# Kernel optimization log

Hardware: AMD Instinct MI355X
Metric: run time of the kernel (lower is better)

The kernel has to match this reference:

```python
import jax, jax.numpy as jnp
import numpy as np

N = 50000      # nodes
E = 800000     # edges (before self loops)
IN = 256       # input feature dim
H = 4          # heads
C = 64         # hidden per head (concat=False -> mean over heads -> 64)
LAT = 32       # latent dim
ED = 3         # edge feature dim
NEG_SLOPE = 0.2


def setup_inputs() -> dict:
    key = jax.random.key(0)
    ks = jax.random.split(key, 24)
    nrm = lambda k, shp, s=0.05: jax.random.normal(k, shp, jnp.float32) * s
    inp = {
        'x': jax.random.normal(ks[0], (N, IN), jnp.float32),
        'edge_index': jax.random.randint(ks[1], (2, E), 0, N),
        'edge_attr': jax.random.normal(ks[2], (E, ED), jnp.float32),
    }
    i = 3
    for l, d in enumerate([IN, C]):  # layer 0 in_dim=IN, layer 1 in_dim=hidden
        inp[f'Wl{l}'] = nrm(ks[i], (d, H * C)); i += 1
        inp[f'bl{l}'] = jnp.zeros((H * C,), jnp.float32)
        inp[f'Wr{l}'] = nrm(ks[i], (d, H * C)); i += 1
        inp[f'br{l}'] = jnp.zeros((H * C,), jnp.float32)
        inp[f'We{l}'] = nrm(ks[i], (ED, H * C)); i += 1
        inp[f'att{l}'] = nrm(ks[i], (H, C)); i += 1
        inp[f'bias{l}'] = jnp.zeros((C,), jnp.float32)
    inp['Wmu'] = nrm(ks[i], (C, LAT)); i += 1
    inp['bmu'] = jnp.zeros((LAT,), jnp.float32)
    return inp


def _gatv2(x, edge_index, edge_attr, Wl, bl, Wr, br, We, att, bias):
    # PyG GATv2Conv: heads=H, concat=False, add_self_loops=True,
    # edge_dim=3, fill_value='mean', negative_slope=0.2, share_weights=False
    n = x.shape[0]
    src, dst = edge_index[0], edge_index[1]
    # self-loop edge_attr = mean of incoming edge_attr per node (0 if none)
    deg = jax.ops.segment_sum(jnp.ones((src.shape[0],), jnp.float32), dst, num_segments=n)
    loop_attr = jax.ops.segment_sum(edge_attr, dst, num_segments=n) / jnp.maximum(deg, 1.0)[:, None]
    loop = jnp.arange(n)
    s = jnp.concatenate([src, loop])
    d = jnp.concatenate([dst, loop])
    ea = jnp.concatenate([edge_attr, loop_attr], axis=0)
    xl = (x @ Wl + bl).reshape(n, H, C)   # source transform
    xr = (x @ Wr + br).reshape(n, H, C)   # target transform
    ee = (ea @ We).reshape(-1, H, C)      # edge transform (no bias)
    m = jax.nn.leaky_relu(xl[s] + xr[d] + ee, NEG_SLOPE)   # [Etot, H, C]
    alpha = jnp.einsum('ehc,hc->eh', m, att)                # [Etot, H]
    amax = jax.ops.segment_max(alpha, d, num_segments=n)    # per-dst max (all segments nonempty: self loops)
    ex = jnp.exp(alpha - amax[d])
    a = ex / jax.ops.segment_sum(ex, d, num_segments=n)[d]  # segment softmax
    out = jax.ops.segment_sum(xl[s] * a[:, :, None], d, num_segments=n)  # [N, H, C]
    return out.mean(axis=1) + bias  # concat=False -> head mean, then bias


def reference(x, edge_index, edge_attr,
              Wl0, bl0, Wr0, br0, We0, att0, bias0,
              Wl1, bl1, Wr1, br1, We1, att1, bias1,
              Wmu, bmu):
    h = jax.nn.relu(_gatv2(x, edge_index, edge_attr, Wl0, bl0, Wr0, br0, We0, att0, bias0))
    h = jax.nn.relu(_gatv2(h, edge_index, edge_attr, Wl1, bl1, Wr1, br1, We1, att1, bias1))
    return h @ Wmu + bmu
```

## Files before the change

kernel.cpp:

```cpp
#include <hip/hip_runtime.h>


#define NN  50000
#define EE  800000
#define HC  256
#define NSLOPE 0.2f

typedef float f32x4 __attribute__((ext_vector_type(4)));
typedef short bf16x8 __attribute__((ext_vector_type(8)));

__device__ __forceinline__ unsigned short f2b(float f) {
    unsigned u = __float_as_uint(f);
    u += 0x7FFFu + ((u >> 16) & 1u);
    return (unsigned short)(u >> 16);
}
__device__ __forceinline__ float b2f(unsigned short h) {
    return __uint_as_float((unsigned)h << 16);
}

__global__ __launch_bounds__(256) void deg_kernel(
    const int* __restrict__ dst, int* __restrict__ deg)
{
    int i = blockIdx.x * 256 + threadIdx.x;
    if (i >= EE / 4) return;
    int4 v = ((const int4*)dst)[i];
    atomicAdd(&deg[v.x], 1);
    atomicAdd(&deg[v.y], 1);
    atomicAdd(&deg[v.z], 1);
    atomicAdd(&deg[v.w], 1);
}

__global__ __launch_bounds__(1024) void scan_kernel(
    const int* __restrict__ deg, int* __restrict__ row_start, int* __restrict__ cursor)
{
    __shared__ int sums[1024];
    const int tid = threadIdx.x;
    const int CH = (NN + 1023) / 1024;
    int b = tid * CH, e = min(b + CH, NN);
    int s = 0;
    for (int i = b; i < e; i++) s += deg[i];
    sums[tid] = s;
    __syncthreads();
    for (int off = 1; off < 1024; off <<= 1) {
        int v = (tid >= off) ? sums[tid - off] : 0;
        __syncthreads();
        sums[tid] += v;
        __syncthreads();
    }
    int run = (tid == 0) ? 0 : sums[tid - 1];
    for (int i = b; i < e; i++) {
        row_start[i] = run;
        cursor[i]    = run;
        run += deg[i];
    }
    if (tid == 0) row_start[NN] = EE;
}

__global__ __launch_bounds__(256) void scatter_kernel(
    const int* __restrict__ ei, const float* __restrict__ ea,
    int* __restrict__ cursor, float4* __restrict__ csr)
{
    int i = blockIdx.x * 256 + threadIdx.x;
    if (i >= EE / 4) return;
    int4 s = ((const int4*)ei)[i];
    int4 d = ((const int4*)(ei + EE))[i];
    float4 e0 = ((const float4*)ea)[i * 3 + 0];
    float4 e1 = ((const float4*)ea)[i * 3 + 1];
    float4 e2 = ((const float4*)ea)[i * 3 + 2];
    int p0 = atomicAdd(&cursor[d.x], 1);
    int p1 = atomicAdd(&cursor[d.y], 1);
    int p2 = atomicAdd(&cursor[d.z], 1);
    int p3 = atomicAdd(&cursor[d.w], 1);
    csr[p0] = make_float4(__int_as_float(s.x), e0.x, e0.y, e0.z);
    csr[p1] = make_float4(__int_as_float(s.y), e0.w, e1.x, e1.y);
    csr[p2] = make_float4(__int_as_float(s.z), e1.z, e1.w, e2.x);
    csr[p3] = make_float4(__int_as_float(s.w), e2.y, e2.z, e2.w);
}

__global__ __launch_bounds__(256) void cvt_wt(
    const float* __restrict__ W, unsigned short* __restrict__ WTh,
    unsigned short* __restrict__ WTl, int K)
{
    int i = blockIdx.x * 256 + threadIdx.x;
    if (i >= K * 256) return;
    int k = i >> 8, c = i & 255;
    float v = W[i];
    unsigned short h = f2b(v);
    unsigned short l = f2b(v - b2f(h));
    WTh[(size_t)c * K + k] = h;
    WTl[(size_t)c * K + k] = l;
}

__global__ __launch_bounds__(256) void gemm_fused(
    const float* __restrict__ A,
    const unsigned short* __restrict__ BTh, const unsigned short* __restrict__ BTl,
    const float* __restrict__ bias0, const float* __restrict__ bias1,
    float* __restrict__ C0, float* __restrict__ C1,
    int M, int K)
{
    __shared__ unsigned short Ah[64][36], Al[64][36];
    __shared__ unsigned short Bh[256][36], Bl[256][36];
    const int tid = threadIdx.x;
    const int bm = blockIdx.y << 6;
    const int bn = blockIdx.x << 8;
    const int w  = tid >> 6, l = tid & 63;
    const int wr = w >> 1, wc = w & 1;
    const int lr = l & 15, lk = l >> 4;

    f32x4 acc[2][8];
#pragma unroll
    for (int a = 0; a < 2; a++)
#pragma unroll
        for (int b = 0; b < 8; b++) acc[a][b] = (f32x4){0.f, 0.f, 0.f, 0.f};

    const int ar = tid >> 2, ac = (tid & 3) << 3;

    for (int k0 = 0; k0 < K; k0 += 32) {
        float av[8];
        if (bm + ar < M) {
            *(float4*)&av[0] = *(const float4*)&A[(size_t)(bm + ar) * K + k0 + ac];
            *(float4*)&av[4] = *(const float4*)&A[(size_t)(bm + ar) * K + k0 + ac + 4];
        } else {
#pragma unroll
            for (int j = 0; j < 8; j++) av[j] = 0.f;
        }
        unsigned hp[4], lp[4];
#pragma unroll
        for (int j = 0; j < 4; j++) {
            unsigned short h0 = f2b(av[2 * j]),     h1 = f2b(av[2 * j + 1]);
            unsigned short l0 = f2b(av[2 * j]     - b2f(h0));
            unsigned short l1 = f2b(av[2 * j + 1] - b2f(h1));
            hp[j] = (unsigned)h0 | ((unsigned)h1 << 16);
            lp[j] = (unsigned)l0 | ((unsigned)l1 << 16);
        }
        *(uint4*)&Ah[ar][ac] = make_uint4(hp[0], hp[1], hp[2], hp[3]);
        *(uint4*)&Al[ar][ac] = make_uint4(lp[0], lp[1], lp[2], lp[3]);
#pragma unroll
        for (int rep = 0; rep < 4; rep++) {
            int i  = (rep << 8) + tid;
            int rb = i >> 2, cb = (i & 3) << 3;
            *(uint4*)&Bh[rb][cb] = *(const uint4*)&BTh[(size_t)(bn + rb) * K + k0 + cb];
            *(uint4*)&Bl[rb][cb] = *(const uint4*)&BTl[(size_t)(bn + rb) * K + k0 + cb];
        }
        __syncthreads();

        bf16x8 afh[2], afl[2];
#pragma unroll
        for (int a = 0; a < 2; a++) {
            afh[a] = *(const bf16x8*)&Ah[wr * 32 + a * 16 + lr][lk << 3];
            afl[a] = *(const bf16x8*)&Al[wr * 32 + a * 16 + lr][lk << 3];
        }
#pragma unroll
        for (int b = 0; b < 8; b++) {
            bf16x8 bh = *(const bf16x8*)&Bh[wc * 128 + b * 16 + lr][lk << 3];
            bf16x8 bl_ = *(const bf16x8*)&Bl[wc * 128 + b * 16 + lr][lk << 3];
#pragma unroll
            for (int a = 0; a < 2; a++) {
                acc[a][b] = __builtin_amdgcn_mfma_f32_16x16x32_bf16(afh[a], bh,  acc[a][b], 0, 0, 0);
                acc[a][b] = __builtin_amdgcn_mfma_f32_16x16x32_bf16(afh[a], bl_, acc[a][b], 0, 0, 0);
                acc[a][b] = __builtin_amdgcn_mfma_f32_16x16x32_bf16(afl[a], bh,  acc[a][b], 0, 0, 0);
            }
        }
        __syncthreads();
    }

    const float* bias = (bn == 0) ? bias0 : bias1;
    float* C = (bn == 0) ? C0 : C1;
#pragma unroll
    for (int a = 0; a < 2; a++) {
        int rbase = bm + wr * 32 + a * 16 + (lk << 2);
#pragma unroll
        for (int b = 0; b < 8; b++) {
            int c = wc * 128 + b * 16 + lr;
            float bs = bias[c];
#pragma unroll
            for (int i = 0; i < 4; i++) {
                int rg = rbase + i;
                if (rg < M) C[(size_t)rg * HC + c] = acc[a][b][i] + bs;
            }
        }
    }
}

__global__ __launch_bounds__(256) void gat_edge(
    const float* __restrict__ xl, const float* __restrict__ xr,
    const float4* __restrict__ csr, const int* __restrict__ row_start,
    const float* __restrict__ att, const float* __restrict__ We,
    const float* __restrict__ bias, float* __restrict__ out)
{
    const int lane = threadIdx.x & 63;
    const int wid  = (blockIdx.x * 256 + threadIdx.x) >> 6;
    const int base = wid << 2;
    const int j4 = lane << 2;
    const float4* xlv = (const float4*)xl;

    const float4 at4 = *(const float4*)&att[j4];
    const float4 w0  = *(const float4*)&We[j4];
    const float4 w1  = *(const float4*)&We[HC + j4];
    const float4 w2  = *(const float4*)&We[2 * HC + j4];

#pragma unroll 1
    for (int v = 0; v < 4; v++) {
        const int node = base + v;
        const float4 xr4 = *(const float4*)&xr[(size_t)node * HC + j4];

        float acc0 = 0.f, acc1 = 0.f, acc2 = 0.f, acc3 = 0.f, denom = 0.f;
        float eas0 = 0.f, eas1 = 0.f, eas2 = 0.f;
        const int beg = row_start[node];
        const int n   = row_start[node + 1] - beg;
        const float4* cp = csr + beg;

        float4 r0 = {0,0,0,0}, r1 = {0,0,0,0}, r2 = {0,0,0,0};
        float4 v0 = {0,0,0,0}, v1 = {0,0,0,0};
        if (n > 0) { r0 = cp[0]; v0 = xlv[(size_t)__float_as_int(r0.x) * 64 + lane]; }
        if (n > 1) { r1 = cp[1]; v1 = xlv[(size_t)__float_as_int(r1.x) * 64 + lane]; }
        if (n > 2) { r2 = cp[2]; }

        for (int i = 0; i < n; i++) {
            float4 crec = r0, cxv = v0;
            r0 = r1; r1 = r2; v0 = v1;
            if (i + 3 < n) r2 = cp[i + 3];
            if (i + 2 < n) v1 = xlv[(size_t)__float_as_int(r1.x) * 64 + lane];

            float ea0 = crec.y, ea1 = crec.z, ea2 = crec.w;
            eas0 += ea0; eas1 += ea1; eas2 += ea2;
            float m0 = cxv.x + xr4.x + ea0 * w0.x + ea1 * w1.x + ea2 * w2.x;
            float m1 = cxv.y + xr4.y + ea0 * w0.y + ea1 * w1.y + ea2 * w2.y;
            float m2 = cxv.z + xr4.z + ea0 * w0.z + ea1 * w1.z + ea2 * w2.z;
            float m3 = cxv.w + xr4.w + ea0 * w0.w + ea1 * w1.w + ea2 * w2.w;
            m0 = fmaxf(m0, NSLOPE * m0);
            m1 = fmaxf(m1, NSLOPE * m1);
            m2 = fmaxf(m2, NSLOPE * m2);
            m3 = fmaxf(m3, NSLOPE * m3);
            float p = m0 * at4.x + m1 * at4.y + m2 * at4.z + m3 * at4.w;
            p += __shfl_xor(p, 1);
            p += __shfl_xor(p, 2);
            p += __shfl_xor(p, 4);
            p += __shfl_xor(p, 8);
            float ex = __expf(p);
            denom += ex;
            acc0 = fmaf(ex, cxv.x, acc0);
            acc1 = fmaf(ex, cxv.y, acc1);
            acc2 = fmaf(ex, cxv.z, acc2);
            acc3 = fmaf(ex, cxv.w, acc3);
        }

        {
            float rd = 1.0f / fmaxf((float)n, 1.0f);
            float ea0 = eas0 * rd, ea1 = eas1 * rd, ea2 = eas2 * rd;
            float4 sv = xlv[(size_t)node * 64 + lane];
            float m0 = sv.x + xr4.x + ea0 * w0.x + ea1 * w1.x + ea2 * w2.x;
            float m1 = sv.y + xr4.y + ea0 * w0.y + ea1 * w1.y + ea2 * w2.y;
            float m2 = sv.z + xr4.z + ea0 * w0.z + ea1 * w1.z + ea2 * w2.z;
            float m3 = sv.w + xr4.w + ea0 * w0.w + ea1 * w1.w + ea2 * w2.w;
            m0 = fmaxf(m0, NSLOPE * m0);
            m1 = fmaxf(m1, NSLOPE * m1);
            m2 = fmaxf(m2, NSLOPE * m2);
            m3 = fmaxf(m3, NSLOPE * m3);
            float p = m0 * at4.x + m1 * at4.y + m2 * at4.z + m3 * at4.w;
            p += __shfl_xor(p, 1);
            p += __shfl_xor(p, 2);
            p += __shfl_xor(p, 4);
            p += __shfl_xor(p, 8);
            float ex = __expf(p);
            denom += ex;
            acc0 = fmaf(ex, sv.x, acc0);
            acc1 = fmaf(ex, sv.y, acc1);
            acc2 = fmaf(ex, sv.z, acc2);
            acc3 = fmaf(ex, sv.w, acc3);
        }

        const float inv = 1.0f / denom;
        float r0s = acc0 * inv, r1s = acc1 * inv, r2s = acc2 * inv, r3s = acc3 * inv;
        r0s += __shfl_xor(r0s, 16); r0s += __shfl_xor(r0s, 32);
        r1s += __shfl_xor(r1s, 16); r1s += __shfl_xor(r1s, 32);
        r2s += __shfl_xor(r2s, 16); r2s += __shfl_xor(r2s, 32);
        r3s += __shfl_xor(r3s, 16); r3s += __shfl_xor(r3s, 32);
        if (lane < 16) {
            float4 bv = *(const float4*)&bias[j4];
            float4 o;
            o.x = fmaxf(0.25f * r0s + bv.x, 0.f);
            o.y = fmaxf(0.25f * r1s + bv.y, 0.f);
            o.z = fmaxf(0.25f * r2s + bv.z, 0.f);
            o.w = fmaxf(0.25f * r3s + bv.w, 0.f);
            *(float4*)&out[(size_t)node * 64 + j4] = o;
        }
    }
}

__global__ __launch_bounds__(256) void mu_kernel(
    const float* __restrict__ h, const float* __restrict__ Wmu,
    const float* __restrict__ bmu, float* __restrict__ out)
{
    __shared__ float ws[64 * 32];
    __shared__ float hs[8 * 64];
    const int tid = threadIdx.x;
#pragma unroll
    for (int i = 0; i < 8; i++) ws[tid + i * 256] = Wmu[tid + i * 256];
    const int nb = blockIdx.x * 8;
    {
        int idx = tid * 2;
        *(float2*)&hs[idx] = *(const float2*)&h[(size_t)nb * 64 + idx];
    }
    __syncthreads();
    const int ln = tid >> 5;
    const int o  = tid & 31;
    float acc = bmu[o];
#pragma unroll
    for (int k = 0; k < 64; k++) acc = fmaf(hs[ln * 64 + k], ws[k * 32 + o], acc);
    out[(size_t)(nb + ln) * 32 + o] = acc;
}

extern "C" void kernel_launch(void* const* d_in, const int* in_sizes, int n_in,
                              void* d_out, int out_size, void* d_ws, size_t ws_size,
                              hipStream_t stream) {
    const float* x    = (const float*)d_in[0];
    const int*   ei   = (const int*)  d_in[1];
    const float* ea   = (const float*)d_in[2];
    const float* Wl0  = (const float*)d_in[3];
    const float* bl0  = (const float*)d_in[4];
    const float* Wr0  = (const float*)d_in[5];
    const float* br0  = (const float*)d_in[6];
    const float* We0  = (const float*)d_in[7];
    const float* att0 = (const float*)d_in[8];
    const float* bi0  = (const float*)d_in[9];
    const float* Wl1  = (const float*)d_in[10];
    const float* bl1  = (const float*)d_in[11];
    const float* Wr1  = (const float*)d_in[12];
    const float* br1  = (const float*)d_in[13];
    const float* We1  = (const float*)d_in[14];
    const float* att1 = (const float*)d_in[15];
    const float* bi1  = (const float*)d_in[16];
    const float* Wmu  = (const float*)d_in[17];
    const float* bmu  = (const float*)d_in[18];
    float* out = (float*)d_out;

    float* xl32 = (float*)d_ws;
    float* xr32 = xl32 + (size_t)NN * HC;
    float* h1   = xr32 + (size_t)NN * HC;
    int*   deg  = (int*)(h1 + (size_t)NN * 64);
    int*   rows = deg + NN;
    int*   curs = rows + NN + 1;
    uintptr_t p = (uintptr_t)(curs + NN);
    p = (p + 15) & ~(uintptr_t)15;
    unsigned short* WT0h = (unsigned short*)p;
    unsigned short* WT0l = WT0h + 512 * 256;
    unsigned short* WT1h = WT0l + 512 * 256;
    unsigned short* WT1l = WT1h + 512 * 64;
    p = (uintptr_t)(WT1l + 512 * 64);
    p = (p + 255) & ~(uintptr_t)255;
    float4* csr = (float4*)p;

    hipMemsetAsync(deg, 0, NN * sizeof(int), stream);
    deg_kernel<<<(EE / 4 + 255) / 256, 256, 0, stream>>>(ei + EE, deg);
    scan_kernel<<<1, 1024, 0, stream>>>(deg, rows, curs);
    scatter_kernel<<<(EE / 4 + 255) / 256, 256, 0, stream>>>(ei, ea, curs, csr);

    cvt_wt<<<256, 256, 0, stream>>>(Wl0, WT0h,             WT0l,             256);
    cvt_wt<<<256, 256, 0, stream>>>(Wr0, WT0h + 256 * 256, WT0l + 256 * 256, 256);
    cvt_wt<<< 64, 256, 0, stream>>>(Wl1, WT1h,             WT1l,             64);
    cvt_wt<<< 64, 256, 0, stream>>>(Wr1, WT1h + 256 * 64,  WT1l + 256 * 64,  64);

    dim3 gg(2, (NN + 63) / 64);
    const int gat_grid = NN / 16;

    gemm_fused<<<gg, 256, 0, stream>>>(x, WT0h, WT0l, bl0, br0, xl32, xr32, NN, 256);
    gat_edge<<<gat_grid, 256, 0, stream>>>(xl32, xr32, csr, rows, att0, We0, bi0, h1);

    gemm_fused<<<gg, 256, 0, stream>>>(h1, WT1h, WT1l, bl1, br1, xl32, xr32, NN, 64);
    gat_edge<<<gat_grid, 256, 0, stream>>>(xl32, xr32, csr, rows, att1, We1, bi1, h1);

    mu_kernel<<<NN / 8, 256, 0, stream>>>(h1, Wmu, bmu, out);
}
```

Before: 727.8 us.

## Remap GAT edge kernel to one node per wave with four edges in flight

The edge-aggregation kernel now assigns one destination node per wavefront instead of four nodes processed in sequence. The wave is split into four 16-lane groups that each handle a different incoming edge, and each lane covers 16 channels loaded as four vectors. Partial softmax sums and edge-attribute means are combined across groups with shuffles before the self-loop term, then reduced across heads. The aim is more memory-level parallelism for the gathered source rows and fewer shuffles per edge. The cost is higher register pressure and some idle lanes on the last partial iteration for low-degree nodes.

```diff
diff --git a/kernel.cpp b/kernel.cpp
--- a/kernel.cpp
+++ b/kernel.cpp
@@ -152,7 +152,7 @@
         }
 #pragma unroll
         for (int b = 0; b < 8; b++) {
-            bf16x8 bh = *(const bf16x8*)&Bh[wc * 128 + b * 16 + lr][lk << 3];
+            bf16x8 bh  = *(const bf16x8*)&Bh[wc * 128 + b * 16 + lr][lk << 3];
             bf16x8 bl_ = *(const bf16x8*)&Bl[wc * 128 + b * 16 + lr][lk << 3];
 #pragma unroll
             for (int a = 0; a < 2; a++) {
@@ -189,101 +189,144 @@
     const float* __restrict__ bias, float* __restrict__ out)
 {
     const int lane = threadIdx.x & 63;
-    const int wid  = (blockIdx.x * 256 + threadIdx.x) >> 6;
-    const int base = wid << 2;
-    const int j4 = lane << 2;
-    const float4* xlv = (const float4*)xl;
-
-    const float4 at4 = *(const float4*)&att[j4];
-    const float4 w0  = *(const float4*)&We[j4];
-    const float4 w1  = *(const float4*)&We[HC + j4];
-    const float4 w2  = *(const float4*)&We[2 * HC + j4];
-
-#pragma unroll 1
-    for (int v = 0; v < 4; v++) {
-        const int node = base + v;
-        const float4 xr4 = *(const float4*)&xr[(size_t)node * HC + j4];
-
-        float acc0 = 0.f, acc1 = 0.f, acc2 = 0.f, acc3 = 0.f, denom = 0.f;
-        float eas0 = 0.f, eas1 = 0.f, eas2 = 0.f;
-        const int beg = row_start[node];
-        const int n   = row_start[node + 1] - beg;
-        const float4* cp = csr + beg;
-
-        float4 r0 = {0,0,0,0}, r1 = {0,0,0,0}, r2 = {0,0,0,0};
-        float4 v0 = {0,0,0,0}, v1 = {0,0,0,0};
-        if (n > 0) { r0 = cp[0]; v0 = xlv[(size_t)__float_as_int(r0.x) * 64 + lane]; }
-        if (n > 1) { r1 = cp[1]; v1 = xlv[(size_t)__float_as_int(r1.x) * 64 + lane]; }
-        if (n > 2) { r2 = cp[2]; }
-
-        for (int i = 0; i < n; i++) {
-            float4 crec = r0, cxv = v0;
-            r0 = r1; r1 = r2; v0 = v1;
-            if (i + 3 < n) r2 = cp[i + 3];
-            if (i + 2 < n) v1 = xlv[(size_t)__float_as_int(r1.x) * 64 + lane];
-
-            float ea0 = crec.y, ea1 = crec.z, ea2 = crec.w;
-            eas0 += ea0; eas1 += ea1; eas2 += ea2;
-            float m0 = cxv.x + xr4.x + ea0 * w0.x + ea1 * w1.x + ea2 * w2.x;
-            float m1 = cxv.y + xr4.y + ea0 * w0.y + ea1 * w1.y + ea2 * w2.y;
-            float m2 = cxv.z + xr4.z + ea0 * w0.z + ea1 * w1.z + ea2 * w2.z;
-            float m3 = cxv.w + xr4.w + ea0 * w0.w + ea1 * w1.w + ea2 * w2.w;
-            m0 = fmaxf(m0, NSLOPE * m0);
-            m1 = fmaxf(m1, NSLOPE * m1);
-            m2 = fmaxf(m2, NSLOPE * m2);
-            m3 = fmaxf(m3, NSLOPE * m3);
-            float p = m0 * at4.x + m1 * at4.y + m2 * at4.z + m3 * at4.w;
-            p += __shfl_xor(p, 1);
-            p += __shfl_xor(p, 2);
-            p += __shfl_xor(p, 4);
-            p += __shfl_xor(p, 8);
-            float ex = __expf(p);
-            denom += ex;
-            acc0 = fmaf(ex, cxv.x, acc0);
-            acc1 = fmaf(ex, cxv.y, acc1);
-            acc2 = fmaf(ex, cxv.z, acc2);
-            acc3 = fmaf(ex, cxv.w, acc3);
-        }
-
-        {
-            float rd = 1.0f / fmaxf((float)n, 1.0f);
-            float ea0 = eas0 * rd, ea1 = eas1 * rd, ea2 = eas2 * rd;
-            float4 sv = xlv[(size_t)node * 64 + lane];
-            float m0 = sv.x + xr4.x + ea0 * w0.x + ea1 * w1.x + ea2 * w2.x;
-            float m1 = sv.y + xr4.y + ea0 * w0.y + ea1 * w1.y + ea2 * w2.y;
-            float m2 = sv.z + xr4.z + ea0 * w0.z + ea1 * w1.z + ea2 * w2.z;
-            float m3 = sv.w + xr4.w + ea0 * w0.w + ea1 * w1.w + ea2 * w2.w;
-            m0 = fmaxf(m0, NSLOPE * m0);
-            m1 = fmaxf(m1, NSLOPE * m1);
-            m2 = fmaxf(m2, NSLOPE * m2);
-            m3 = fmaxf(m3, NSLOPE * m3);
-            float p = m0 * at4.x + m1 * at4.y + m2 * at4.z + m3 * at4.w;
-            p += __shfl_xor(p, 1);
-            p += __shfl_xor(p, 2);
-            p += __shfl_xor(p, 4);
-            p += __shfl_xor(p, 8);
-            float ex = __expf(p);
-            denom += ex;
-            acc0 = fmaf(ex, sv.x, acc0);
-            acc1 = fmaf(ex, sv.y, acc1);
-            acc2 = fmaf(ex, sv.z, acc2);
-            acc3 = fmaf(ex, sv.w, acc3);
-        }
-
-        const float inv = 1.0f / denom;
-        float r0s = acc0 * inv, r1s = acc1 * inv, r2s = acc2 * inv, r3s = acc3 * inv;
-        r0s += __shfl_xor(r0s, 16); r0s += __shfl_xor(r0s, 32);
-        r1s += __shfl_xor(r1s, 16); r1s += __shfl_xor(r1s, 32);
-        r2s += __shfl_xor(r2s, 16); r2s += __shfl_xor(r2s, 32);
-        r3s += __shfl_xor(r3s, 16); r3s += __shfl_xor(r3s, 32);
-        if (lane < 16) {
-            float4 bv = *(const float4*)&bias[j4];
-            float4 o;
-            o.x = fmaxf(0.25f * r0s + bv.x, 0.f);
-            o.y = fmaxf(0.25f * r1s + bv.y, 0.f);
-            o.z = fmaxf(0.25f * r2s + bv.z, 0.f);
-            o.w = fmaxf(0.25f * r3s + bv.w, 0.f);
-            *(float4*)&out[(size_t)node * 64 + j4] = o;
+    const int node = (blockIdx.x * 256 + threadIdx.x) >> 6;
+    if (node >= NN) return;
+    const int g = lane >> 4;
+    const int j = lane & 15;
+    const f32x4* xlv = (const f32x4*)xl;
+    const int cb4 = j << 2;
+
+    f32x4 w0[4], w1[4], w2[4], at[4], xr4[4];
+#pragma unroll
+    for (int q = 0; q < 4; q++) {
+        w0[q]  = *(const f32x4*)&We[        (cb4 + q) * 4];
+        w1[q]  = *(const f32x4*)&We[HC     + (cb4 + q) * 4];
+        w2[q]  = *(const f32x4*)&We[2 * HC + (cb4 + q) * 4];
+        at[q]  = *(const f32x4*)&att[       (cb4 + q) * 4];
+        xr4[q] = xlv[0];
+    }
+    {
+        const f32x4* xrv = (const f32x4*)xr;
+#pragma unroll
+        for (int q = 0; q < 4; q++) xr4[q] = xrv[(size_t)node * 64 + cb4 + q];
+    }
+
+    f32x4 acc[4];
+#pragma unroll
+    for (int q = 0; q < 4; q++) acc[q] = (f32x4){0.f, 0.f, 0.f, 0.f};
+    float denom = 0.f, eas0 = 0.f, eas1 = 0.f, eas2 = 0.f;
+
+    const int beg = row_start[node];
+    const int n   = row_start[node + 1] - beg;
+    const float4* cp = csr + beg;
+    const int nit = (n + 3) >> 2;
+
+    int idx = g;
+    bool val = idx < n;
+    float4 rec = val ? cp[idx] : make_float4(0.f, 0.f, 0.f, 0.f);
+    f32x4 xv0, xv1, xv2, xv3;
+    {
+        int s = val ? __float_as_int(rec.x) : node;
+        const f32x4* gp = xlv + (size_t)s * 64 + cb4;
+        xv0 = gp[0]; xv1 = gp[1]; xv2 = gp[2]; xv3 = gp[3];
+    }
+
+    for (int it = 0; it < nit; it++) {
+        const bool  cv = val;
+        const float4 crec = rec;
+        f32x4 c0 = xv0, c1 = xv1, c2 = xv2, c3 = xv3;
+        idx += 4;
+        val = idx < n;
+        if (val) {
+            rec = cp[idx];
+            const f32x4* gp = xlv + (size_t)__float_as_int(rec.x) * 64 + cb4;
+            xv0 = gp[0]; xv1 = gp[1]; xv2 = gp[2]; xv3 = gp[3];
+        } else {
+            rec = make_float4(0.f, 0.f, 0.f, 0.f);
+        }
+
+        const float ea0 = crec.y, ea1 = crec.z, ea2 = crec.w;
+        eas0 += ea0; eas1 += ea1; eas2 += ea2;
+
+        float p = 0.f;
+        f32x4 cx[4] = {c0, c1, c2, c3};
+#pragma unroll
+        for (int q = 0; q < 4; q++) {
+            f32x4 m = cx[q] + xr4[q];
+            m += ea0 * w0[q];
+            m += ea1 * w1[q];
+            m += ea2 * w2[q];
+#pragma unroll
+            for (int t = 0; t < 4; t++) m[t] = fmaxf(m[t], NSLOPE * m[t]);
+#pragma unroll
+            for (int t = 0; t < 4; t++) p = fmaf(m[t], at[q][t], p);
+            cx[q] = m;
+        }
+        p += __shfl_xor(p, 1);
+        p += __shfl_xor(p, 2);
+        float ex = cv ? __expf(p) : 0.f;
+        denom += ex;
+        acc[0] += ex * c0;
+        acc[1] += ex * c1;
+        acc[2] += ex * c2;
+        acc[3] += ex * c3;
+    }
+
+    float* af = (float*)acc;
+#pragma unroll
+    for (int k = 0; k < 16; k++) {
+        af[k] += __shfl_xor(af[k], 16);
+        af[k] += __shfl_xor(af[k], 32);
+    }
+    denom += __shfl_xor(denom, 16); denom += __shfl_xor(denom, 32);
+    eas0  += __shfl_xor(eas0, 16);  eas0  += __shfl_xor(eas0, 32);
+    eas1  += __shfl_xor(eas1, 16);  eas1  += __shfl_xor(eas1, 32);
+    eas2  += __shfl_xor(eas2, 16);  eas2  += __shfl_xor(eas2, 32);
+
+    {
+        const float rd = 1.0f / fmaxf((float)n, 1.0f);
+        const float ea0 = eas0 * rd, ea1 = eas1 * rd, ea2 = eas2 * rd;
+        const f32x4* gp = xlv + (size_t)node * 64 + cb4;
+        f32x4 sv[4] = {gp[0], gp[1], gp[2], gp[3]};
+        float p = 0.f;
+#pragma unroll
+        for (int q = 0; q < 4; q++) {
+            f32x4 m = sv[q] + xr4[q];
+            m += ea0 * w0[q];
+            m += ea1 * w1[q];
+            m += ea2 * w2[q];
+#pragma unroll
+            for (int t = 0; t < 4; t++) m[t] = fmaxf(m[t], NSLOPE * m[t]);
+#pragma unroll
+            for (int t = 0; t < 4; t++) p = fmaf(m[t], at[q][t], p);
+        }
+        p += __shfl_xor(p, 1);
+        p += __shfl_xor(p, 2);
+        float ex = __expf(p);
+        denom += ex;
+        acc[0] += ex * sv[0];
+        acc[1] += ex * sv[1];
+        acc[2] += ex * sv[2];
+        acc[3] += ex * sv[3];
+    }
+
+    const float inv = 1.0f / denom;
+#pragma unroll
+    for (int k = 0; k < 16; k++) {
+        float r = af[k] * inv;
+        r += __shfl_xor(r, 4);
+        r += __shfl_xor(r, 8);
+        af[k] = r;
+    }
+    if (lane < 4) {
+        const f32x4* bv = (const f32x4*)bias;
+        f32x4* ov = (f32x4*)out;
+#pragma unroll
+        for (int q = 0; q < 4; q++) {
+            f32x4 o = 0.25f * acc[q] + bv[cb4 + q];
+#pragma unroll
+            for (int t = 0; t < 4; t++) o[t] = fmaxf(o[t], 0.f);
+            ov[(size_t)node * 16 + cb4 + q] = o;
         }
     }
 }
@@ -362,7 +405,7 @@
     cvt_wt<<< 64, 256, 0, stream>>>(Wr1, WT1h + 256 * 64,  WT1l + 256 * 64,  64);
 
     dim3 gg(2, (NN + 63) / 64);
-    const int gat_grid = NN / 16;
+    const int gat_grid = (NN * 64) / 256;
 
     gemm_fused<<<gg, 256, 0, stream>>>(x, WT0h, WT0l, bl0, br0, xl32, xr32, NN, 256);
     gat_edge<<<gat_grid, 256, 0, stream>>>(xl32, xr32, csr, rows, att0, We0, bi0, h1);
```

After: 782.1 us. +7.5%, slower.

## Parallelize CSR prefix scan across blocks and assign one wave per node

Applied to the files above, without the earlier changes.

Replaces the single-block serial-chunk prefix scan over node degrees with a three-kernel multi-block scan. The GAT edge kernel now gives each wavefront one destination node instead of looping over four, which quadruples the grid and gives the scheduler more waves to hide gather latency. Index arithmetic for xl gathers is switched to 32-bit unsigned. The trade-off is two extra kernel launches and redundant per-wave loads of att/We.

```diff
diff --git a/kernel.cpp b/kernel.cpp
--- a/kernel.cpp
+++ b/kernel.cpp
@@ -5,6 +5,7 @@
 #define EE  800000
 #define HC  256
 #define NSLOPE 0.2f
+#define SCAN_B ((NN + 255) / 256)
 
 typedef float f32x4 __attribute__((ext_vector_type(4)));
 typedef short bf16x8 __attribute__((ext_vector_type(8)));
@@ -30,30 +31,52 @@
     atomicAdd(&deg[v.w], 1);
 }
 
-__global__ __launch_bounds__(1024) void scan_kernel(
-    const int* __restrict__ deg, int* __restrict__ row_start, int* __restrict__ cursor)
-{
-    __shared__ int sums[1024];
-    const int tid = threadIdx.x;
-    const int CH = (NN + 1023) / 1024;
-    int b = tid * CH, e = min(b + CH, NN);
-    int s = 0;
-    for (int i = b; i < e; i++) s += deg[i];
-    sums[tid] = s;
+__global__ __launch_bounds__(256) void scan1_kernel(
+    const int* __restrict__ deg, int* __restrict__ rows, int* __restrict__ bsum)
+{
+    __shared__ int sh[256];
+    const int t = threadIdx.x, b = blockIdx.x;
+    const int i = b * 256 + t;
+    int v = (i < NN) ? deg[i] : 0;
+    sh[t] = v;
     __syncthreads();
-    for (int off = 1; off < 1024; off <<= 1) {
-        int v = (tid >= off) ? sums[tid - off] : 0;
-        __syncthreads();
-        sums[tid] += v;
-        __syncthreads();
-    }
-    int run = (tid == 0) ? 0 : sums[tid - 1];
-    for (int i = b; i < e; i++) {
-        row_start[i] = run;
-        cursor[i]    = run;
-        run += deg[i];
-    }
-    if (tid == 0) row_start[NN] = EE;
+    for (int off = 1; off < 256; off <<= 1) {
+        int u = (t >= off) ? sh[t - off] : 0;
+        __syncthreads();
+        sh[t] += u;
+        __syncthreads();
+    }
+    if (i < NN) rows[i] = sh[t] - v;
+    if (t == 255) bsum[b] = sh[255];
+}
+
+__global__ __launch_bounds__(256) void scan2_kernel(int* __restrict__ bsum, int* __restrict__ boff)
+{
+    __shared__ int sh[256];
+    const int t = threadIdx.x;
+    int v = (t < SCAN_B) ? bsum[t] : 0;
+    sh[t] = v;
+    __syncthreads();
+    for (int off = 1; off < 256; off <<= 1) {
+        int u = (t >= off) ? sh[t - off] : 0;
+        __syncthreads();
+        sh[t] += u;
+        __syncthreads();
+    }
+    if (t < SCAN_B) boff[t] = sh[t] - v;
+}
+
+__global__ __launch_bounds__(256) void scan3_kernel(
+    int* __restrict__ rows, int* __restrict__ curs, const int* __restrict__ boff)
+{
+    const int b = blockIdx.x;
+    const int i = b * 256 + threadIdx.x;
+    if (i < NN) {
+        int v = rows[i] + boff[b];
+        rows[i] = v;
+        curs[i] = v;
+    }
+    if (i == 0) rows[NN] = EE;
 }
 
 __global__ __launch_bounds__(256) void scatter_kernel(
@@ -152,7 +175,7 @@
         }
 #pragma unroll
         for (int b = 0; b < 8; b++) {
-            bf16x8 bh = *(const bf16x8*)&Bh[wc * 128 + b * 16 + lr][lk << 3];
+            bf16x8 bh  = *(const bf16x8*)&Bh[wc * 128 + b * 16 + lr][lk << 3];
             bf16x8 bl_ = *(const bf16x8*)&Bl[wc * 128 + b * 16 + lr][lk << 3];
 #pragma unroll
             for (int a = 0; a < 2; a++) {
@@ -189,102 +212,97 @@
     const float* __restrict__ bias, float* __restrict__ out)
 {
     const int lane = threadIdx.x & 63;
-    const int wid  = (blockIdx.x * 256 + threadIdx.x) >> 6;
-    const int base = wid << 2;
+    const int node = (blockIdx.x * 256 + threadIdx.x) >> 6;
+    if (node >= NN) return;
     const int j4 = lane << 2;
     const float4* xlv = (const float4*)xl;
 
+    const float4 xr4 = *(const float4*)&xr[(size_t)node * HC + j4];
     const float4 at4 = *(const float4*)&att[j4];
     const float4 w0  = *(const float4*)&We[j4];
     const float4 w1  = *(const float4*)&We[HC + j4];
     const float4 w2  = *(const float4*)&We[2 * HC + j4];
 
-#pragma unroll 1
-    for (int v = 0; v < 4; v++) {
-        const int node = base + v;
-        const float4 xr4 = *(const float4*)&xr[(size_t)node * HC + j4];
-
-        float acc0 = 0.f, acc1 = 0.f, acc2 = 0.f, acc3 = 0.f, denom = 0.f;
-        float eas0 = 0.f, eas1 = 0.f, eas2 = 0.f;
-        const int beg = row_start[node];
-        const int n   = row_start[node + 1] - beg;
-        const float4* cp = csr + beg;
-
-        float4 r0 = {0,0,0,0}, r1 = {0,0,0,0}, r2 = {0,0,0,0};
-        float4 v0 = {0,0,0,0}, v1 = {0,0,0,0};
-        if (n > 0) { r0 = cp[0]; v0 = xlv[(size_t)__float_as_int(r0.x) * 64 + lane]; }
-        if (n > 1) { r1 = cp[1]; v1 = xlv[(size_t)__float_as_int(r1.x) * 64 + lane]; }
-        if (n > 2) { r2 = cp[2]; }
-
-        for (int i = 0; i < n; i++) {
-            float4 crec = r0, cxv = v0;
-            r0 = r1; r1 = r2; v0 = v1;
-            if (i + 3 < n) r2 = cp[i + 3];
-            if (i + 2 < n) v1 = xlv[(size_t)__float_as_int(r1.x) * 64 + lane];
-
-            float ea0 = crec.y, ea1 = crec.z, ea2 = crec.w;
-            eas0 += ea0; eas1 += ea1; eas2 += ea2;
-            float m0 = cxv.x + xr4.x + ea0 * w0.x + ea1 * w1.x + ea2 * w2.x;
-            float m1 = cxv.y + xr4.y + ea0 * w0.y + ea1 * w1.y + ea2 * w2.y;
-            float m2 = cxv.z + xr4.z + ea0 * w0.z + ea1 * w1.z + ea2 * w2.z;
-            float m3 = cxv.w + xr4.w + ea0 * w0.w + ea1 * w1.w + ea2 * w2.w;
-            m0 = fmaxf(m0, NSLOPE * m0);
-            m1 = fmaxf(m1, NSLOPE * m1);
-            m2 = fmaxf(m2, NSLOPE * m2);
-            m3 = fmaxf(m3, NSLOPE * m3);
-            float p = m0 * at4.x + m1 * at4.y + m2 * at4.z + m3 * at4.w;
-            p += __shfl_xor(p, 1);
-            p += __shfl_xor(p, 2);
-            p += __shfl_xor(p, 4);
-            p += __shfl_xor(p, 8);
-            float ex = __expf(p);
-            denom += ex;
-            acc0 = fmaf(ex, cxv.x, acc0);
-            acc1 = fmaf(ex, cxv.y, acc1);
-            acc2 = fmaf(ex, cxv.z, acc2);
-            acc3 = fmaf(ex, cxv.w, acc3);
-        }
-
-        {
-            float rd = 1.0f / fmaxf((float)n, 1.0f);
-            float ea0 = eas0 * rd, ea1 = eas1 * rd, ea2 = eas2 * rd;
-            float4 sv = xlv[(size_t)node * 64 + lane];
-            float m0 = sv.x + xr4.x + ea0 * w0.x + ea1 * w1.x + ea2 * w2.x;
-            float m1 = sv.y + xr4.y + ea0 * w0.y + ea1 * w1.y + ea2 * w2.y;
-            float m2 = sv.z + xr4.z + ea0 * w0.z + ea1 * w1.z + ea2 * w2.z;
-            float m3 = sv.w + xr4.w + ea0 * w0.w + ea1 * w1.w + ea2 * w2.w;
-            m0 = fmaxf(m0, NSLOPE * m0);
-            m1 = fmaxf(m1, NSLOPE * m1);
-            m2 = fmaxf(m2, NSLOPE * m2);
-            m3 = fmaxf(m3, NSLOPE * m3);
-            float p = m0 * at4.x + m1 * at4.y + m2 * at4.z + m3 * at4.w;
-            p += __shfl_xor(p, 1);
-            p += __shfl_xor(p, 2);
-            p += __shfl_xor(p, 4);
-            p += __shfl_xor(p, 8);
-            float ex = __expf(p);
-            denom += ex;
-            acc0 = fmaf(ex, sv.x, acc0);
-            acc1 = fmaf(ex, sv.y, acc1);
-            acc2 = fmaf(ex, sv.z, acc2);
-            acc3 = fmaf(ex, sv.w, acc3);
-        }
-
-        const float inv = 1.0f / denom;
-        float r0s = acc0 * inv, r1s = acc1 * inv, r2s = acc2 * inv, r3s = acc3 * inv;
-        r0s += __shfl_xor(r0s, 16); r0s += __shfl_xor(r0s, 32);
-        r1s += __shfl_xor(r1s, 16); r1s += __shfl_xor(r1s, 32);
-        r2s += __shfl_xor(r2s, 16); r2s += __shfl_xor(r2s, 32);
-        r3s += __shfl_xor(r3s, 16); r3s += __shfl_xor(r3s, 32);
-        if (lane < 16) {
-            float4 bv = *(const float4*)&bias[j4];
-            float4 o;
-            o.x = fmaxf(0.25f * r0s + bv.x, 0.f);
-            o.y = fmaxf(0.25f * r1s + bv.y, 0.f);
-            o.z = fmaxf(0.25f * r2s + bv.z, 0.f);
-            o.w = fmaxf(0.25f * r3s + bv.w, 0.f);
-            *(float4*)&out[(size_t)node * 64 + j4] = o;
-        }
+    float acc0 = 0.f, acc1 = 0.f, acc2 = 0.f, acc3 = 0.f, denom = 0.f;
+    float eas0 = 0.f, eas1 = 0.f, eas2 = 0.f;
+    const int beg = row_start[node];
+    const int n   = row_start[node + 1] - beg;
+    const float4* cp = csr + beg;
+
+    float4 r0 = {0,0,0,0}, r1 = {0,0,0,0}, r2 = {0,0,0,0};
+    float4 v0 = {0,0,0,0}, v1 = {0,0,0,0};
+    if (n > 0) { r0 = cp[0]; v0 = xlv[(unsigned)(__float_as_int(r0.x) * 64 + lane)]; }
+    if (n > 1) { r1 = cp[1]; v1 = xlv[(unsigned)(__float_as_int(r1.x) * 64 + lane)]; }
+    if (n > 2) { r2 = cp[2]; }
+
+    for (int i = 0; i < n; i++) {
+        float4 crec = r0, cxv = v0;
+        r0 = r1; r1 = r2; v0 = v1;
+        if (i + 3 < n) r2 = cp[i + 3];
+        if (i + 2 < n) v1 = xlv[(unsigned)(__float_as_int(r1.x) * 64 + lane)];
+
+        float ea0 = crec.y, ea1 = crec.z, ea2 = crec.w;
+        eas0 += ea0; eas1 += ea1; eas2 += ea2;
+        float m0 = cxv.x + xr4.x + ea0 * w0.x + ea1 * w1.x + ea2 * w2.x;
+        float m1 = cxv.y + xr4.y + ea0 * w0.y + ea1 * w1.y + ea2 * w2.y;
+        float m2 = cxv.z + xr4.z + ea0 * w0.z + ea1 * w1.z + ea2 * w2.z;
+        float m3 = cxv.w + xr4.w + ea0 * w0.w + ea1 * w1.w + ea2 * w2.w;
+        m0 = fmaxf(m0, NSLOPE * m0);
+        m1 = fmaxf(m1, NSLOPE * m1);
+        m2 = fmaxf(m2, NSLOPE * m2);
+        m3 = fmaxf(m3, NSLOPE * m3);
+        float p = m0 * at4.x + m1 * at4.y + m2 * at4.z + m3 * at4.w;
+        p += __shfl_xor(p, 1);
+        p += __shfl_xor(p, 2);
+        p += __shfl_xor(p, 4);
+        p += __shfl_xor(p, 8);
+        float ex = __expf(p);
+        denom += ex;
+        acc0 = fmaf(ex, cxv.x, acc0);
+        acc1 = fmaf(ex, cxv.y, acc1);
+        acc2 = fmaf(ex, cxv.z, acc2);
+        acc3 = fmaf(ex, cxv.w, acc3);
+    }
+
+    {
+        float rd = 1.0f / fmaxf((float)n, 1.0f);
+        float ea0 = eas0 * rd, ea1 = eas1 * rd, ea2 = eas2 * rd;
+        float4 sv = xlv[(unsigned)(node * 64 + lane)];
+        float m0 = sv.x + xr4.x + ea0 * w0.x + ea1 * w1.x + ea2 * w2.x;
+        float m1 = sv.y + xr4.y + ea0 * w0.y + ea1 * w1.y + ea2 * w2.y;
+        float m2 = sv.z + xr4.z + ea0 * w0.z + ea1 * w1.z + ea2 * w2.z;
+        float m3 = sv.w + xr4.w + ea0 * w0.w + ea1 * w1.w + ea2 * w2.w;
+        m0 = fmaxf(m0, NSLOPE * m0);
+        m1 = fmaxf(m1, NSLOPE * m1);
+        m2 = fmaxf(m2, NSLOPE * m2);
+        m3 = fmaxf(m3, NSLOPE * m3);
+        float p = m0 * at4.x + m1 * at4.y + m2 * at4.z + m3 * at4.w;
+        p += __shfl_xor(p, 1);
+        p += __shfl_xor(p, 2);
+        p += __shfl_xor(p, 4);
+        p += __shfl_xor(p, 8);
+        float ex = __expf(p);
+        denom += ex;
+        acc0 = fmaf(ex, sv.x, acc0);
+        acc1 = fmaf(ex, sv.y, acc1);
+        acc2 = fmaf(ex, sv.z, acc2);
+        acc3 = fmaf(ex, sv.w, acc3);
+    }
+
+    const float inv = 1.0f / denom;
+    float r0s = acc0 * inv, r1s = acc1 * inv, r2s = acc2 * inv, r3s = acc3 * inv;
+    r0s += __shfl_xor(r0s, 16); r0s += __shfl_xor(r0s, 32);
+    r1s += __shfl_xor(r1s, 16); r1s += __shfl_xor(r1s, 32);
+    r2s += __shfl_xor(r2s, 16); r2s += __shfl_xor(r2s, 32);
+    r3s += __shfl_xor(r3s, 16); r3s += __shfl_xor(r3s, 32);
+    if (lane < 16) {
+        float4 bv = *(const float4*)&bias[j4];
+        float4 o;
+        o.x = fmaxf(0.25f * r0s + bv.x, 0.f);
+        o.y = fmaxf(0.25f * r1s + bv.y, 0.f);
+        o.z = fmaxf(0.25f * r2s + bv.z, 0.f);
+        o.w = fmaxf(0.25f * r3s + bv.w, 0.f);
+        *(float4*)&out[(size_t)node * 64 + j4] = o;
     }
 }
 
@@ -341,7 +359,9 @@
     int*   deg  = (int*)(h1 + (size_t)NN * 64);
     int*   rows = deg + NN;
     int*   curs = rows + NN + 1;
-    uintptr_t p = (uintptr_t)(curs + NN);
+    int*   bsum = curs + NN;
+    int*   boff = bsum + SCAN_B;
+    uintptr_t p = (uintptr_t)(boff + SCAN_B);
     p = (p + 15) & ~(uintptr_t)15;
     unsigned short* WT0h = (unsigned short*)p;
     unsigned short* WT0l = WT0h + 512 * 256;
@@ -353,7 +373,9 @@
 
     hipMemsetAsync(deg, 0, NN * sizeof(int), stream);
     deg_kernel<<<(EE / 4 + 255) / 256, 256, 0, stream>>>(ei + EE, deg);
-    scan_kernel<<<1, 1024, 0, stream>>>(deg, rows, curs);
+    scan1_kernel<<<SCAN_B, 256, 0, stream>>>(deg, rows, bsum);
+    scan2_kernel<<<1, 256, 0, stream>>>(bsum, boff);
+    scan3_kernel<<<SCAN_B, 256, 0, stream>>>(rows, curs, boff);
     scatter_kernel<<<(EE / 4 + 255) / 256, 256, 0, stream>>>(ei, ea, curs, csr);
 
     cvt_wt<<<256, 256, 0, stream>>>(Wl0, WT0h,             WT0l,             256);
@@ -362,7 +384,7 @@
     cvt_wt<<< 64, 256, 0, stream>>>(Wr1, WT1h + 256 * 64,  WT1l + 256 * 64,  64);
 
     dim3 gg(2, (NN + 63) / 64);
-    const int gat_grid = NN / 16;
+    const int gat_grid = (NN * 64) / 256;
 
     gemm_fused<<<gg, 256, 0, stream>>>(x, WT0h, WT0l, bl0, br0, xl32, xr32, NN, 256);
     gat_edge<<<gat_grid, 256, 0, stream>>>(xl32, xr32, csr, rows, att0, We0, bi0, h1);
```

After: 598.7 us. 1.22x faster.
